# Performance work log

Measured on AMD Instinct MI355X. Metric: run time of the kernel, lower is better.

The kernel has to match this reference:

```python
import jax, jax.numpy as jnp
import numpy as np

N_NODES = 50000
N_EDGES = 800000
IN_DIM = 9
HIDDEN = 256
N_CAND = 4096


def setup_inputs() -> dict:
    key = jax.random.key(0)
    ks = jax.random.split(key, 12)
    x = jax.random.normal(ks[0], (N_NODES, IN_DIM), dtype=jnp.float32)
    edge_index = jax.random.randint(ks[1], (2, N_EDGES), 0, N_NODES, dtype=jnp.int64)
    candidate_indices = jax.random.randint(ks[2], (N_CAND,), 0, N_NODES, dtype=jnp.int64)
    # GCNConv weights (glorot-ish scale) and biases
    W1 = jax.random.normal(ks[3], (IN_DIM, HIDDEN), dtype=jnp.float32) / np.sqrt(IN_DIM)
    b1 = jnp.zeros((HIDDEN,), dtype=jnp.float32)
    W2 = jax.random.normal(ks[4], (HIDDEN, HIDDEN), dtype=jnp.float32) / np.sqrt(HIDDEN)
    b2 = jnp.zeros((HIDDEN,), dtype=jnp.float32)
    # score head: Linear(hidden,hidden) -> Tanh -> Linear(hidden,1)
    Wh1 = jax.random.normal(ks[5], (HIDDEN, HIDDEN), dtype=jnp.float32) / np.sqrt(HIDDEN)
    bh1 = jnp.zeros((HIDDEN,), dtype=jnp.float32)
    Wh2 = jax.random.normal(ks[6], (HIDDEN, 1), dtype=jnp.float32) / np.sqrt(HIDDEN)
    bh2 = jnp.zeros((1,), dtype=jnp.float32)
    return {"x": x, "W1": W1, "b1": b1, "W2": W2, "b2": b2,
            "Wh1": Wh1, "bh1": bh1, "Wh2": Wh2, "bh2": bh2,
            "edge_index": edge_index, "candidate_indices": candidate_indices}


def _gcn_norm(edge_index, n_nodes):
    # PyG GCNConv default: add self-loops, symmetric normalization D^-1/2 (A+I) D^-1/2
    loop = jnp.arange(n_nodes, dtype=edge_index.dtype)
    src = jnp.concatenate([edge_index[0], loop])
    dst = jnp.concatenate([edge_index[1], loop])
    deg = jax.ops.segment_sum(jnp.ones_like(dst, dtype=jnp.float32), dst,
                              num_segments=n_nodes)
    dinv = jnp.where(deg > 0, jax.lax.rsqrt(deg), 0.0)
    norm = dinv[src] * dinv[dst]  # [E+N]
    return src, dst, norm


def _gcn_layer(h, src, dst, norm, W, b, n_nodes):
    m = h @ W                              # [N, H] dense GEMM first (fewer edge features)
    msg = m[src] * norm[:, None]           # gather + scale: [E+N, H]
    agg = jax.ops.segment_sum(msg, dst, num_segments=n_nodes)  # scatter-add
    return jax.nn.relu(agg + b)


def reference(x, W1, b1, W2, b2, Wh1, bh1, Wh2, bh2, edge_index, candidate_indices):
    n = x.shape[0]
    src, dst, norm = _gcn_norm(edge_index, n)
    h = _gcn_layer(x, src, dst, norm, W1, b1, n)
    h = _gcn_layer(h, src, dst, norm, W2, b2, n)
    cand_h = h[candidate_indices]                       # [K, H]
    scores = (jnp.tanh(cand_h @ Wh1 + bh1) @ Wh2 + bh2).squeeze(-1)  # [K]
    return scores
```

## Files before the change

### kernel.cpp

```cpp
#include <hip/hip_runtime.h>
#include <math.h>

#define N_NODES 50000
#define N_EDGES 800000
#define IN_DIM  9
#define HIDDEN  256
#define N_CAND  4096

#define SCAN_TPB 256
#define SCAN_NB  ((N_NODES + SCAN_TPB - 1) / SCAN_TPB)


__global__ void hist_kernel(const int* __restrict__ dst, int* __restrict__ cnt) {
    int e = blockIdx.x * blockDim.x + threadIdx.x;
    if (e < N_EDGES) atomicAdd(&cnt[dst[e]], 1);
}

__global__ __launch_bounds__(SCAN_TPB) void scan1_kernel(const int* __restrict__ cnt,
                                                         int* __restrict__ row_ptr,
                                                         int* __restrict__ blockSums) {
    __shared__ int s[SCAN_TPB];
    int t = threadIdx.x;
    int i = blockIdx.x * SCAN_TPB + t;
    int v = (i < N_NODES) ? cnt[i] : 0;
    s[t] = v;
    __syncthreads();
#pragma unroll
    for (int off = 1; off < SCAN_TPB; off <<= 1) {
        int u = (t >= off) ? s[t - off] : 0;
        __syncthreads();
        s[t] += u;
        __syncthreads();
    }
    if (i < N_NODES) row_ptr[i] = s[t] - v;
    if (t == SCAN_TPB - 1) blockSums[blockIdx.x] = s[t];
}

__global__ __launch_bounds__(SCAN_TPB) void scan2_kernel(const int* __restrict__ blockSums,
                                                         int* __restrict__ blockOff,
                                                         int* __restrict__ row_ptr) {
    __shared__ int s[SCAN_TPB];
    int t = threadIdx.x;
    int v = (t < SCAN_NB) ? blockSums[t] : 0;
    s[t] = v;
    __syncthreads();
#pragma unroll
    for (int off = 1; off < SCAN_TPB; off <<= 1) {
        int u = (t >= off) ? s[t - off] : 0;
        __syncthreads();
        s[t] += u;
        __syncthreads();
    }
    if (t < SCAN_NB) blockOff[t] = s[t] - v;
    if (t == SCAN_TPB - 1) row_ptr[N_NODES] = s[t];
}

__global__ __launch_bounds__(SCAN_TPB) void scan3_kernel(const int* __restrict__ cnt,
                                                         const int* __restrict__ blockOff,
                                                         int* __restrict__ row_ptr,
                                                         float* __restrict__ dinv) {
    int i = blockIdx.x * SCAN_TPB + threadIdx.x;
    if (i < N_NODES) {
        row_ptr[i] += blockOff[blockIdx.x];
        dinv[i] = 1.0f / sqrtf((float)(cnt[i] + 1));
    }
}

__global__ void fill_kernel(const int* __restrict__ srcv, const int* __restrict__ dstv,
                            const int* __restrict__ row_ptr, int* __restrict__ cur,
                            int* __restrict__ col) {
    int e = blockIdx.x * blockDim.x + threadIdx.x;
    if (e < N_EDGES) {
        int d = dstv[e];
        int pos = row_ptr[d] + atomicAdd(&cur[d], 1);
        col[pos] = srcv[e];
    }
}


__global__ __launch_bounds__(256) void aggx_kernel(const float* __restrict__ x,
                                                   const int* __restrict__ row_ptr,
                                                   const int* __restrict__ col,
                                                   const float* __restrict__ dinv,
                                                   float* __restrict__ ax) {
    int tid  = threadIdx.x;
    int node = blockIdx.x * 16 + (tid >> 4);
    int l    = tid & 15;
    if (node >= N_NODES) return;

    float a[IN_DIM];
#pragma unroll
    for (int d = 0; d < IN_DIM; ++d) a[d] = 0.f;

    int beg = row_ptr[node], end = row_ptr[node + 1];
    for (int j = beg + l; j < end; j += 16) {
        int s = col[j];
        float w = dinv[s];
        const float* xs = x + (size_t)s * IN_DIM;
#pragma unroll
        for (int d = 0; d < IN_DIM; ++d) a[d] += w * xs[d];
    }

#pragma unroll
    for (int m = 8; m >= 1; m >>= 1) {
#pragma unroll
        for (int d = 0; d < IN_DIM; ++d) a[d] += __shfl_xor(a[d], m);
    }

    float di = dinv[node];
    const float* xi = x + (size_t)node * IN_DIM;
    float o[IN_DIM];
#pragma unroll
    for (int d = 0; d < IN_DIM; ++d) o[d] = di * (di * xi[d] + a[d]);

    float v = o[0];
    if (l == 1) v = o[1];
    if (l == 2) v = o[2];
    if (l == 3) v = o[3];
    if (l == 4) v = o[4];
    if (l == 5) v = o[5];
    if (l == 6) v = o[6];
    if (l == 7) v = o[7];
    if (l == 8) v = o[8];
    if (l < IN_DIM) ax[(size_t)node * IN_DIM + l] = v;
}


#define NPB 8
__global__ __launch_bounds__(256) void h1_kernel(const float* __restrict__ ax,
                                                 const float* __restrict__ W1,
                                                 const float* __restrict__ b1,
                                                 float* __restrict__ h1) {
    int n0 = blockIdx.x * NPB;
    int c = threadIdx.x;
    __shared__ float s[NPB][IN_DIM];
    if (c < NPB * IN_DIM) s[c / IN_DIM][c % IN_DIM] = ax[(size_t)n0 * IN_DIM + c];
    __syncthreads();
    float w[IN_DIM];
#pragma unroll
    for (int k = 0; k < IN_DIM; ++k) w[k] = W1[k * HIDDEN + c];
    float b = b1[c];
#pragma unroll
    for (int r = 0; r < NPB; ++r) {
        float acc = b;
#pragma unroll
        for (int k = 0; k < IN_DIM; ++k) acc += s[r][k] * w[k];
        h1[(size_t)(n0 + r) * HIDDEN + c] = fmaxf(acc, 0.f);
    }
}


__global__ __launch_bounds__(256) void aggc_kernel(const float* __restrict__ h1,
                                                   const int* __restrict__ cand,
                                                   const int* __restrict__ row_ptr,
                                                   const int* __restrict__ col,
                                                   const float* __restrict__ dinv,
                                                   float* __restrict__ g) {
    int k = blockIdx.x * 4 + (threadIdx.x >> 6);
    if (k >= N_CAND) return;
    int lane = threadIdx.x & 63;
    int node = cand[k];
    const float di = dinv[node];
    float4 v = ((const float4*)(h1 + (size_t)node * HIDDEN))[lane];
    float4 acc = make_float4(di * v.x, di * v.y, di * v.z, di * v.w);
    int j = row_ptr[node], end = row_ptr[node + 1];
    for (; j < end; ++j) {
        int s = col[j];
        float w = dinv[s];
        float4 mv = ((const float4*)(h1 + (size_t)s * HIDDEN))[lane];
        acc.x += w * mv.x; acc.y += w * mv.y; acc.z += w * mv.z; acc.w += w * mv.w;
    }
    float4 o = make_float4(di * acc.x, di * acc.y, di * acc.z, di * acc.w);
    ((float4*)(g + (size_t)k * HIDDEN))[lane] = o;
}


#define CPB 4
__global__ __launch_bounds__(256) void head_fused_kernel(const float* __restrict__ g,
                                                         const float* __restrict__ W2,
                                                         const float* __restrict__ b2,
                                                         const float* __restrict__ Wh1,
                                                         const float* __restrict__ bh1,
                                                         const float* __restrict__ Wh2,
                                                         const float* __restrict__ bh2,
                                                         float* __restrict__ out) {
    __shared__ float A[CPB][HIDDEN];
    __shared__ float B[CPB][HIDDEN];
    __shared__ float red[CPB][4];
    int k0 = blockIdx.x * CPB;
    int c = threadIdx.x;

#pragma unroll
    for (int r = 0; r < CPB; ++r) A[r][c] = g[(size_t)(k0 + r) * HIDDEN + c];
    __syncthreads();

    float acc[CPB];
    {
        float b = b2[c];
#pragma unroll
        for (int r = 0; r < CPB; ++r) acc[r] = b;
        for (int i = 0; i < HIDDEN; i += 4) {
            float w0 = W2[(i + 0) * HIDDEN + c];
            float w1 = W2[(i + 1) * HIDDEN + c];
            float w2 = W2[(i + 2) * HIDDEN + c];
            float w3 = W2[(i + 3) * HIDDEN + c];
#pragma unroll
            for (int r = 0; r < CPB; ++r) {
                float4 a = *(const float4*)&A[r][i];
                acc[r] += a.x * w0 + a.y * w1 + a.z * w2 + a.w * w3;
            }
        }
#pragma unroll
        for (int r = 0; r < CPB; ++r) B[r][c] = fmaxf(acc[r], 0.f);
    }
    __syncthreads();

    {
        float b = bh1[c];
#pragma unroll
        for (int r = 0; r < CPB; ++r) acc[r] = b;
        for (int i = 0; i < HIDDEN; i += 4) {
            float w0 = Wh1[(i + 0) * HIDDEN + c];
            float w1 = Wh1[(i + 1) * HIDDEN + c];
            float w2 = Wh1[(i + 2) * HIDDEN + c];
            float w3 = Wh1[(i + 3) * HIDDEN + c];
#pragma unroll
            for (int r = 0; r < CPB; ++r) {
                float4 a = *(const float4*)&B[r][i];
                acc[r] += a.x * w0 + a.y * w1 + a.z * w2 + a.w * w3;
            }
        }
        float w2c = Wh2[c];
#pragma unroll
        for (int r = 0; r < CPB; ++r) acc[r] = tanhf(acc[r]) * w2c;
    }

#pragma unroll
    for (int r = 0; r < CPB; ++r) {
        float v = acc[r];
#pragma unroll
        for (int off = 32; off > 0; off >>= 1) v += __shfl_down(v, off);
        if ((c & 63) == 0) red[r][c >> 6] = v;
    }
    __syncthreads();
    if (c < CPB) out[k0 + c] = red[c][0] + red[c][1] + red[c][2] + red[c][3] + bh2[0];
}


extern "C" void kernel_launch(void* const* d_in, const int* in_sizes, int n_in,
                              void* d_out, int out_size, void* d_ws, size_t ws_size,
                              hipStream_t stream) {
    const float* x   = (const float*)d_in[0];
    const float* W1  = (const float*)d_in[1];
    const float* b1  = (const float*)d_in[2];
    const float* W2  = (const float*)d_in[3];
    const float* b2  = (const float*)d_in[4];
    const float* Wh1 = (const float*)d_in[5];
    const float* bh1 = (const float*)d_in[6];
    const float* Wh2 = (const float*)d_in[7];
    const float* bh2 = (const float*)d_in[8];
    const int* edge_index = (const int*)d_in[9];
    const int* cand       = (const int*)d_in[10];
    float* out = (float*)d_out;

    char* ws = (char*)d_ws;
    size_t off = 0;
    auto alloc = [&](size_t bytes) -> void* {
        void* p = ws + off;
        off += (bytes + 255) & ~(size_t)255;
        return p;
    };
    int*   cnt       = (int*)alloc((size_t)N_NODES * 4);
    int*   row_ptr   = (int*)alloc((size_t)(N_NODES + 1) * 4);
    int*   cur       = (int*)alloc((size_t)N_NODES * 4);
    float* dinv      = (float*)alloc((size_t)N_NODES * 4);
    int*   blockSums = (int*)alloc((size_t)SCAN_NB * 4);
    int*   blockOff  = (int*)alloc((size_t)SCAN_NB * 4);
    int*   col       = (int*)alloc((size_t)N_EDGES * 4);
    float* ax        = (float*)alloc((size_t)N_NODES * IN_DIM * 4);
    float* h1        = (float*)alloc((size_t)N_NODES * HIDDEN * 4);
    float* g         = (float*)alloc((size_t)N_CAND * HIDDEN * 4);

    const int* src = edge_index;
    const int* dst = edge_index + N_EDGES;

    hipMemsetAsync(cnt, 0, (size_t)N_NODES * 4, stream);
    hipMemsetAsync(cur, 0, (size_t)N_NODES * 4, stream);

    const int EB = (N_EDGES + 255) / 256;
    hist_kernel<<<EB, 256, 0, stream>>>(dst, cnt);
    scan1_kernel<<<SCAN_NB, SCAN_TPB, 0, stream>>>(cnt, row_ptr, blockSums);
    scan2_kernel<<<1, SCAN_TPB, 0, stream>>>(blockSums, blockOff, row_ptr);
    scan3_kernel<<<SCAN_NB, SCAN_TPB, 0, stream>>>(cnt, blockOff, row_ptr, dinv);
    fill_kernel<<<EB, 256, 0, stream>>>(src, dst, row_ptr, cur, col);

    aggx_kernel<<<(N_NODES + 15) / 16, 256, 0, stream>>>(x, row_ptr, col, dinv, ax);
    h1_kernel<<<N_NODES / NPB, 256, 0, stream>>>(ax, W1, b1, h1);
    aggc_kernel<<<(N_CAND + 3) / 4, 256, 0, stream>>>(h1, cand, row_ptr, col, dinv, g);
    head_fused_kernel<<<N_CAND / CPB, 256, 0, stream>>>(g, W2, b2, Wh1, bh1, Wh2, bh2, out);
}
```

Measured before the change: 264.8 us.

## Transpose head weights, vectorize CSR fill, and seed cursors from row_ptr

scan3 now writes the final row offsets into the cursor array, which removes one memset and the extra row_ptr read in the fill step. The fill kernel processes four edges per thread using int4 loads. Two new transpose kernels store W2 and Wh1 transposed so the fused head kernel can read each weight row with float4 loads. The risk is that in the transposed layout, neighbouring threads read addresses one full row apart, so the head's weight loads are no longer coalesced across the wavefront.

```diff
diff --git a/kernel.cpp b/kernel.cpp
--- a/kernel.cpp
+++ b/kernel.cpp
@@ -58,23 +58,46 @@
 __global__ __launch_bounds__(SCAN_TPB) void scan3_kernel(const int* __restrict__ cnt,
                                                          const int* __restrict__ blockOff,
                                                          int* __restrict__ row_ptr,
+                                                         int* __restrict__ cur,
                                                          float* __restrict__ dinv) {
     int i = blockIdx.x * SCAN_TPB + threadIdx.x;
     if (i < N_NODES) {
-        row_ptr[i] += blockOff[blockIdx.x];
+        int rp = row_ptr[i] + blockOff[blockIdx.x];
+        row_ptr[i] = rp;
+        cur[i] = rp;
         dinv[i] = 1.0f / sqrtf((float)(cnt[i] + 1));
     }
 }
 
 __global__ void fill_kernel(const int* __restrict__ srcv, const int* __restrict__ dstv,
-                            const int* __restrict__ row_ptr, int* __restrict__ cur,
-                            int* __restrict__ col) {
-    int e = blockIdx.x * blockDim.x + threadIdx.x;
-    if (e < N_EDGES) {
-        int d = dstv[e];
-        int pos = row_ptr[d] + atomicAdd(&cur[d], 1);
-        col[pos] = srcv[e];
-    }
+                            int* __restrict__ cur, int* __restrict__ col) {
+    int base = (blockIdx.x * blockDim.x + threadIdx.x) * 4;
+    if (base >= N_EDGES) return;
+    int4 d4 = *(const int4*)(dstv + base);
+    int4 s4 = *(const int4*)(srcv + base);
+    int p0 = atomicAdd(&cur[d4.x], 1);
+    int p1 = atomicAdd(&cur[d4.y], 1);
+    int p2 = atomicAdd(&cur[d4.z], 1);
+    int p3 = atomicAdd(&cur[d4.w], 1);
+    col[p0] = s4.x;
+    col[p1] = s4.y;
+    col[p2] = s4.z;
+    col[p3] = s4.w;
+}
+
+
+__global__ __launch_bounds__(256) void transpose256_kernel(const float* __restrict__ in,
+                                                           float* __restrict__ out) {
+    __shared__ float tile[32][33];
+    int bx = blockIdx.x & 7, by = blockIdx.x >> 3;
+    int tx = threadIdx.x & 31, ty = threadIdx.x >> 5;
+#pragma unroll
+    for (int k = 0; k < 4; ++k)
+        tile[ty + 8 * k][tx] = in[(by * 32 + ty + 8 * k) * HIDDEN + bx * 32 + tx];
+    __syncthreads();
+#pragma unroll
+    for (int k = 0; k < 4; ++k)
+        out[(bx * 32 + ty + 8 * k) * HIDDEN + by * 32 + tx] = tile[tx][ty + 8 * k];
 }
 
 
@@ -177,9 +200,9 @@
 
 #define CPB 4
 __global__ __launch_bounds__(256) void head_fused_kernel(const float* __restrict__ g,
-                                                         const float* __restrict__ W2,
+                                                         const float* __restrict__ w2t,
                                                          const float* __restrict__ b2,
-                                                         const float* __restrict__ Wh1,
+                                                         const float* __restrict__ wh1t,
                                                          const float* __restrict__ bh1,
                                                          const float* __restrict__ Wh2,
                                                          const float* __restrict__ bh2,
@@ -199,15 +222,13 @@
         float b = b2[c];
 #pragma unroll
         for (int r = 0; r < CPB; ++r) acc[r] = b;
+        const float* wrow = w2t + (size_t)c * HIDDEN;
         for (int i = 0; i < HIDDEN; i += 4) {
-            float w0 = W2[(i + 0) * HIDDEN + c];
-            float w1 = W2[(i + 1) * HIDDEN + c];
-            float w2 = W2[(i + 2) * HIDDEN + c];
-            float w3 = W2[(i + 3) * HIDDEN + c];
+            float4 w = *(const float4*)(wrow + i);
 #pragma unroll
             for (int r = 0; r < CPB; ++r) {
                 float4 a = *(const float4*)&A[r][i];
-                acc[r] += a.x * w0 + a.y * w1 + a.z * w2 + a.w * w3;
+                acc[r] += a.x * w.x + a.y * w.y + a.z * w.z + a.w * w.w;
             }
         }
 #pragma unroll
@@ -219,15 +240,13 @@
         float b = bh1[c];
 #pragma unroll
         for (int r = 0; r < CPB; ++r) acc[r] = b;
+        const float* wrow = wh1t + (size_t)c * HIDDEN;
         for (int i = 0; i < HIDDEN; i += 4) {
-            float w0 = Wh1[(i + 0) * HIDDEN + c];
-            float w1 = Wh1[(i + 1) * HIDDEN + c];
-            float w2 = Wh1[(i + 2) * HIDDEN + c];
-            float w3 = Wh1[(i + 3) * HIDDEN + c];
+            float4 w = *(const float4*)(wrow + i);
 #pragma unroll
             for (int r = 0; r < CPB; ++r) {
                 float4 a = *(const float4*)&B[r][i];
-                acc[r] += a.x * w0 + a.y * w1 + a.z * w2 + a.w * w3;
+                acc[r] += a.x * w.x + a.y * w.y + a.z * w.z + a.w * w.w;
             }
         }
         float w2c = Wh2[c];
@@ -280,22 +299,26 @@
     float* ax        = (float*)alloc((size_t)N_NODES * IN_DIM * 4);
     float* h1        = (float*)alloc((size_t)N_NODES * HIDDEN * 4);
     float* g         = (float*)alloc((size_t)N_CAND * HIDDEN * 4);
+    float* w2t       = (float*)alloc((size_t)HIDDEN * HIDDEN * 4);
+    float* wh1t      = (float*)alloc((size_t)HIDDEN * HIDDEN * 4);
 
     const int* src = edge_index;
     const int* dst = edge_index + N_EDGES;
 
     hipMemsetAsync(cnt, 0, (size_t)N_NODES * 4, stream);
-    hipMemsetAsync(cur, 0, (size_t)N_NODES * 4, stream);
 
     const int EB = (N_EDGES + 255) / 256;
     hist_kernel<<<EB, 256, 0, stream>>>(dst, cnt);
     scan1_kernel<<<SCAN_NB, SCAN_TPB, 0, stream>>>(cnt, row_ptr, blockSums);
     scan2_kernel<<<1, SCAN_TPB, 0, stream>>>(blockSums, blockOff, row_ptr);
-    scan3_kernel<<<SCAN_NB, SCAN_TPB, 0, stream>>>(cnt, blockOff, row_ptr, dinv);
-    fill_kernel<<<EB, 256, 0, stream>>>(src, dst, row_ptr, cur, col);
+    scan3_kernel<<<SCAN_NB, SCAN_TPB, 0, stream>>>(cnt, blockOff, row_ptr, cur, dinv);
+    fill_kernel<<<(N_EDGES / 4 + 255) / 256, 256, 0, stream>>>(src, dst, cur, col);
+
+    transpose256_kernel<<<64, 256, 0, stream>>>(W2, w2t);
+    transpose256_kernel<<<64, 256, 0, stream>>>(Wh1, wh1t);
 
     aggx_kernel<<<(N_NODES + 15) / 16, 256, 0, stream>>>(x, row_ptr, col, dinv, ax);
     h1_kernel<<<N_NODES / NPB, 256, 0, stream>>>(ax, W1, b1, h1);
     aggc_kernel<<<(N_CAND + 3) / 4, 256, 0, stream>>>(h1, cand, row_ptr, col, dinv, g);
-    head_fused_kernel<<<N_CAND / CPB, 256, 0, stream>>>(g, W2, b2, Wh1, bh1, Wh2, bh2, out);
-}
+    head_fused_kernel<<<N_CAND / CPB, 256, 0, stream>>>(g, w2t, b2, wh1t, bh1, Wh2, bh2, out);
+}
```

Measured after the change: 291.7 us. 1.1x slower.
